# Performance work log

Hardware: AMD Instinct MI355X
Metric: run time of the kernel (lower is better)

## Reference

```python
import jax, jax.numpy as jnp
import numpy as np

NUM_CLASSES = 81
TOP_K = 200
CONF_THRESH = 0.01
NMS_THRESH = 0.45
VAR0, VAR1 = 0.1, 0.2  # SSD Config['variance']


def decode(loc, priors):
    # loc: [..., P, 4], priors: [P, 4] (cx, cy, w, h)
    cxcy = priors[:, :2] + loc[..., :2] * VAR0 * priors[:, 2:]
    wh = priors[:, 2:] * jnp.exp(loc[..., 2:] * VAR1)
    x1y1 = cxcy - wh * 0.5
    x2y2 = x1y1 + wh
    return jnp.concatenate([x1y1, x2y2], axis=-1)  # [..., P, 4] xyxy


def nms_class(boxes, scores):
    # boxes: [P, 4], scores: [P] -> [TOP_K, 5] rows of (score, x1, y1, x2, y2)
    K = TOP_K
    masked = jnp.where(scores > CONF_THRESH, scores, -jnp.inf)
    top_scores, idx = jax.lax.top_k(masked, K)          # descending
    cand = boxes[idx]                                   # [K, 4]
    valid = jnp.isfinite(top_scores)
    x1, y1, x2, y2 = cand[:, 0], cand[:, 1], cand[:, 2], cand[:, 3]
    area = (x2 - x1) * (y2 - y1)
    iw = jnp.maximum(jnp.minimum(x2[:, None], x2[None, :]) - jnp.maximum(x1[:, None], x1[None, :]), 0.0)
    ih = jnp.maximum(jnp.minimum(y2[:, None], y2[None, :]) - jnp.maximum(y1[:, None], y1[None, :]), 0.0)
    inter = iw * ih
    union = area[:, None] + area[None, :] - inter
    iou = jnp.where(union > 0, inter / jnp.where(union > 0, union, 1.0), 0.0)  # [K, K]
    ar = jnp.arange(K)

    def step(suppressed, i):
        kept = valid[i] & ~suppressed[i]
        suppressed = suppressed | (kept & (iou[i] > NMS_THRESH) & (ar > i))
        return suppressed, kept

    _, keep = jax.lax.scan(step, jnp.zeros(K, dtype=bool), ar)  # [K] bool
    rows = jnp.concatenate([jnp.where(valid, top_scores, 0.0)[:, None], cand], axis=1)  # [K, 5]
    # compact kept rows to the front (score-descending order), zeros after
    tgt = jnp.where(keep, jnp.cumsum(keep) - 1, K)
    out = jnp.zeros((K + 1, 5), rows.dtype).at[tgt].set(rows)[:K]
    return out


def detect(loc_data, conf_data, prior_data):
    boxes = decode(loc_data, prior_data)                 # [B, P, 4]
    conf = jnp.transpose(conf_data, (0, 2, 1))           # [B, C, P]
    per_image = jax.vmap(nms_class, in_axes=(None, 0))   # over classes
    out = jax.vmap(per_image, in_axes=(0, 0))(boxes, conf)  # [B, C, K, 5]
    out = out.at[:, 0].set(0.0)  # background class skipped (cl starts at 1)
    return out


def setup_inputs() -> dict:
    key = jax.random.key(0)
    k1, k2, k3 = jax.random.split(key, 3)
    B, P, C = 32, 24564, NUM_CLASSES
    loc_data = jax.random.normal(k1, (B, P, 4), dtype=jnp.float32)
    conf_data = jax.random.uniform(k2, (B, P, C), dtype=jnp.float32)
    prior_data = jax.random.uniform(k3, (P, 4), dtype=jnp.float32)
    return {"loc_data": loc_data, "conf_data": conf_data, "prior_data": prior_data}


def reference(loc_data, conf_data, prior_data):
    return detect(loc_data, conf_data, prior_data)
```

## Files before the change

kernel.cpp:

```cpp
#include <hip/hip_runtime.h>
#include <hip/hip_bf16.h>
#include <math.h>

constexpr int B_ = 32;
constexpr int P_ = 24564;
constexpr int C_ = 81;
constexpr int K_ = 200;

constexpr int NCH = 64;
constexpr int CPR = 384;
constexpr int SCAP = 1024;
constexpr int CAP  = 512;
constexpr float T_SEL = 0.9869f;

__global__ __launch_bounds__(256) void k_filter(const float* __restrict__ conf,
                                                unsigned long long* __restrict__ cand,
                                                unsigned* __restrict__ cnt,
                                                unsigned* __restrict__ bflag) {
    __shared__ unsigned long long skey[SCAP];
    __shared__ unsigned short scls[SCAP];
    __shared__ unsigned scnt[C_], sbase[C_], scnt2[C_];
    __shared__ unsigned sn;
    const int bid = blockIdx.x;
    const int b = bid / NCH, ch = bid % NCH;
    const int tid = threadIdx.x;

    for (int i = tid; i < C_; i += 256) { scnt[i] = 0; scnt2[i] = 0; }
    if (tid == 0) sn = 0;
    __syncthreads();

    const int p0 = ch * CPR;
    const int rows = min(CPR, P_ - p0);
    const float* slab = conf + ((size_t)b * P_ + (size_t)p0) * C_;
    const int n4 = rows * C_ / 4;
    for (int g = tid; g < n4; g += 256) {
        float4 v = ((const float4*)slab)[g];
        int e = g * 4;
        int c = e % C_;
        int pl = e / C_;
        float s[4] = {v.x, v.y, v.z, v.w};
#pragma unroll
        for (int j = 0; j < 4; ++j) {
            int cj = c + j, pj = pl;
            if (cj >= C_) { cj -= C_; pj += 1; }
            float sv = s[j];
            if (sv > T_SEL && cj != 0) {
                unsigned pos = atomicAdd(&sn, 1u);
                if (pos < (unsigned)SCAP) {
                    unsigned pg = (unsigned)(p0 + pj);
                    skey[pos] = ((unsigned long long)__float_as_uint(sv) << 32) | (~pg);
                    scls[pos] = (unsigned short)cj;
                    atomicAdd(&scnt[cj], 1u);
                } else {
                    bflag[b] = 1u;
                }
            }
        }
    }
    __syncthreads();
    if (tid < C_) sbase[tid] = scnt[tid] ? atomicAdd(&cnt[b * C_ + tid], scnt[tid]) : 0u;
    __syncthreads();
    const int m = (int)min(sn, (unsigned)SCAP);
    for (int i = tid; i < m; i += 256) {
        int c = scls[i];
        unsigned pos = sbase[c] + atomicAdd(&scnt2[c], 1u);
        if (pos < (unsigned)CAP)
            cand[((size_t)(b * C_ + c)) * CAP + pos] = skey[i];
    }
}

__global__ __launch_bounds__(256) void k_nms(const unsigned long long* __restrict__ cand,
                                             const unsigned* __restrict__ cnt,
                                             const unsigned* __restrict__ bflag,
                                             const float* __restrict__ conf,
                                             const float* __restrict__ loc,
                                             const float* __restrict__ prior,
                                             float* __restrict__ out) {
#pragma clang fp contract(off)
    __shared__ __align__(16) unsigned long long masks[K_][4];
    __shared__ __align__(16) unsigned long long top[256];
    __shared__ __align__(16) float4 bbox[K_];
    __shared__ float sc[K_], bar[K_];
    __shared__ unsigned char vflag[K_];
    __shared__ unsigned long long keepw[4];
    __shared__ unsigned kpre[4];
    __shared__ unsigned long long sh_prefix;
    __shared__ unsigned sh_rank, sh_cnt2, sh_cut, sh_fat;

    unsigned long long* buf = &masks[0][0];
    unsigned* rs_hist = (unsigned*)&masks[128][0];
    unsigned* rs_sf   = (unsigned*)&masks[160][0];

    const int bid = blockIdx.x;
    const int b = bid / C_, c = bid % C_;
    const int tid = threadIdx.x;
    const int lane = tid & 63;
    float* obase = out + ((size_t)(b * C_ + c)) * (K_ * 5);

    if (c == 0) {
        float4 z = make_float4(0.f, 0.f, 0.f, 0.f);
        for (int i = tid; i < K_ * 5 / 4; i += 256) ((float4*)obase)[i] = z;
        return;
    }

    const int task = b * C_ + c;
    const unsigned long long* crow = cand + (size_t)task * CAP;
    const unsigned cn = cnt[task];
    const bool fb = (bflag[b] != 0u) || (cn < (unsigned)K_) || (cn > (unsigned)CAP);

    int n;
    int snum = 0;
    bool fat = false;
    if (!fb) {
        n = (int)cn;
        const unsigned long long k1 = (tid < n)       ? crow[tid]       : 0ull;
        const unsigned long long k2 = (tid + 256 < n) ? crow[tid + 256] : 0ull;
        if (n <= 256) {
            top[tid] = k1;
            snum = n;
            __syncthreads();
        } else {
            rs_hist[tid] = 0u;
            top[tid] = 0ull;
            __syncthreads();
            atomicAdd(&rs_hist[(unsigned)((k1 >> 43) & 255ull)], 1u);
            if (tid + 256 < n)
                atomicAdd(&rs_hist[(unsigned)((k2 >> 43) & 255ull)], 1u);
            __syncthreads();
            if (tid < 64) {
                const int l = tid;
                uint4 h = *(const uint4*)&rs_hist[l * 4];
                unsigned s3 = h.w;
                unsigned s2 = h.z + s3;
                unsigned s1 = h.y + s2;
                unsigned s0 = h.x + s1;
                unsigned acc = s0;
                for (int off = 1; off < 64; off <<= 1) {
                    unsigned o = __shfl_down(acc, off, 64);
                    if (l + off < 64) acc += o;
                }
                const unsigned suf_after = acc - s0;
                unsigned long long bal = __ballot(s0 + suf_after >= (unsigned)K_);
                int hl = 63 - __builtin_clzll(bal);
                if (l == hl) {
                    int k; unsigned sufk;
                    if      (s3 + suf_after >= (unsigned)K_) { k = 3; sufk = s3 + suf_after; }
                    else if (s2 + suf_after >= (unsigned)K_) { k = 2; sufk = s2 + suf_after; }
                    else if (s1 + suf_after >= (unsigned)K_) { k = 1; sufk = s1 + suf_after; }
                    else                                     { k = 0; sufk = s0 + suf_after; }
                    sh_cut = (unsigned)(l * 4 + k);
                    sh_fat = (sufk > 256u) ? 1u : 0u;
                    sh_cnt2 = 0u;
                }
            }
            __syncthreads();
            fat = (sh_fat != 0u);
            if (!fat) {
                const unsigned cut = sh_cut;
                {
                    bool q = ((unsigned)((k1 >> 43) & 255ull) >= cut);
                    unsigned long long bal = __ballot(q);
                    unsigned pre = (unsigned)__popcll(bal & ((1ull << lane) - 1ull));
                    unsigned wb = 0;
                    if (lane == 0) {
                        unsigned cw = (unsigned)__popcll(bal);
                        if (cw) wb = atomicAdd(&sh_cnt2, cw);
                    }
                    wb = (unsigned)__shfl((int)wb, 0, 64);
                    if (q) top[wb + pre] = k1;
                }
                {
                    bool q = (tid + 256 < n) && ((unsigned)((k2 >> 43) & 255ull) >= cut);
                    unsigned long long bal = __ballot(q);
                    unsigned pre = (unsigned)__popcll(bal & ((1ull << lane) - 1ull));
                    unsigned wb = 0;
                    if (lane == 0) {
                        unsigned cw = (unsigned)__popcll(bal);
                        if (cw) wb = atomicAdd(&sh_cnt2, cw);
                    }
                    wb = (unsigned)__shfl((int)wb, 0, 64);
                    if (q) top[wb + pre] = k2;
                }
                __syncthreads();
                snum = (int)sh_cnt2;
            } else {
                buf[tid] = k1;
                buf[tid + 256] = k2;
                __syncthreads();
            }
        }
    } else {
        for (int i = tid; i < CAP; i += 256) buf[i] = 0ull;
        const float* col = conf + (size_t)b * P_ * C_ + c;
        unsigned lc = 0;
        for (int p = tid; p < P_; p += 256)
            if (col[(size_t)p * C_] > 0.01f) lc++;
        rs_sf[tid] = lc;
        __syncthreads();
        for (int off = 128; off > 0; off >>= 1) {
            if (tid < off) rs_sf[tid] += rs_sf[tid + off];
            __syncthreads();
        }
        const unsigned total = rs_sf[0];
        unsigned long long t200v = 1ull;
        if (total > (unsigned)K_) {
            if (tid == 0) { sh_prefix = 0ull; sh_rank = (unsigned)K_; }
            __syncthreads();
            for (int d = 7; d >= 0; --d) {
                rs_hist[tid] = 0;
                __syncthreads();
                const unsigned long long pref = sh_prefix;
                const unsigned rank = sh_rank;
                for (int p = tid; p < P_; p += 256) {
                    float sv = col[(size_t)p * C_];
                    if (sv > 0.01f) {
                        unsigned long long key =
                            ((unsigned long long)__float_as_uint(sv) << 32) | (~(unsigned)p);
                        bool match = (d == 7) || (((key ^ pref) >> ((d + 1) * 8)) == 0ull);
                        if (match) atomicAdd(&rs_hist[(unsigned)((key >> (d * 8)) & 255ull)], 1u);
                    }
                }
                __syncthreads();
                rs_sf[tid] = rs_hist[tid];
                __syncthreads();
                for (int off = 1; off < 256; off <<= 1) {
                    unsigned v2 = (tid + off < 256) ? rs_sf[tid + off] : 0u;
                    __syncthreads();
                    rs_sf[tid] += v2;
                    __syncthreads();
                }
                if (rs_sf[tid] >= rank && (tid == 255 || rs_sf[tid + 1] < rank)) {
                    sh_prefix = pref | ((unsigned long long)tid << (d * 8));
                    sh_rank = rank - ((tid == 255) ? 0u : rs_sf[tid + 1]);
                }
                __syncthreads();
            }
            t200v = sh_prefix;
        }
        if (tid == 0) sh_cnt2 = 0;
        __syncthreads();
        for (int p = tid; p < P_; p += 256) {
            float sv = col[(size_t)p * C_];
            if (sv > 0.01f) {
                unsigned long long key =
                    ((unsigned long long)__float_as_uint(sv) << 32) | (~(unsigned)p);
                if (key >= t200v) {
                    unsigned pos = atomicAdd(&sh_cnt2, 1u);
                    if (pos < (unsigned)CAP) buf[pos] = key;
                }
            }
        }
        __syncthreads();
        n = (int)min(sh_cnt2, (unsigned)CAP);
        top[tid] = (tid < n) ? buf[tid] : 0ull;
        snum = n;
        __syncthreads();
    }

    const int nsel = min(n, K_);

    auto decode_to = [&](unsigned long long key, int r) {
        unsigned ub = (unsigned)(key >> 32);
        unsigned p = ~((unsigned)key);
        float score = __uint_as_float(ub);
        bool v = ((ub & 0x7F800000u) != 0x7F800000u);
        const float4 l4 = ((const float4*)loc)[(size_t)b * P_ + p];
        const float4 p4 = ((const float4*)prior)[p];
        float cx = p4.x + (l4.x * 0.1f) * p4.z;
        float cy = p4.y + (l4.y * 0.1f) * p4.w;
        float w  = p4.z * expf(l4.z * 0.2f);
        float h  = p4.w * expf(l4.w * 0.2f);
        float x1 = cx - w * 0.5f;
        float y1 = cy - h * 0.5f;
        float x2 = x1 + w;
        float y2 = y1 + h;
        bbox[r] = make_float4(x1, y1, x2, y2);
        sc[r] = score;
        bar[r] = (x2 - x1) * (y2 - y1);
        vflag[r] = v ? (unsigned char)1 : (unsigned char)0;
    };

    if (!fat) {
        const unsigned long long k = top[tid];
        int r = 0;
        const int mm = (snum + 3) & ~3;
        for (int i = 0; i < mm; i += 4) {
            ulonglong2 a = *(const ulonglong2*)&top[i];
            ulonglong2 d = *(const ulonglong2*)&top[i + 2];
            r += (a.x > k) + (a.y > k) + (d.x > k) + (d.y > k);
        }
        if (k != 0ull && r < K_) decode_to(k, r);
    } else {
        const unsigned long long k1 = buf[tid];
        const unsigned long long k2 = buf[tid + 256];
        int r1 = 0, r2 = 0;
        for (int i = 0; i < CAP; i += 4) {
            ulonglong2 a = *(const ulonglong2*)&buf[i];
            ulonglong2 d = *(const ulonglong2*)&buf[i + 2];
            r1 += (a.x > k1) + (a.y > k1) + (d.x > k1) + (d.y > k1);
            r2 += (a.x > k2) + (a.y > k2) + (d.x > k2) + (d.y > k2);
        }
        if (k1 != 0ull && r1 < K_) decode_to(k1, r1);
        if (k2 != 0ull && r2 < K_) decode_to(k2, r2);
    }
    if (tid >= nsel && tid < K_) {
        bbox[tid] = make_float4(1e30f, 1e30f, 1e30f, 1e30f);
        sc[tid] = 0.f; bar[tid] = 0.f; vflag[tid] = 0;
    }
    __syncthreads();

    const double M_IOU = 0.5 * ((double)__uint_as_float(0x3EE66666u) +
                                (double)__uint_as_float(0x3EE66667u));
    const int nv = nsel;
    const int wid = tid >> 6;

    float4 jb[4]; float jar[4];
#pragma unroll
    for (int w = 0; w < 4; ++w) {
        int j = w * 64 + lane;
        bool in = (j < K_);
        jb[w]  = in ? bbox[j] : make_float4(1e30f, 1e30f, 1e30f, 1e30f);
        jar[w] = in ? bar[j] : 0.f;
    }

    for (int idx = tid; idx < K_ * 4; idx += 256) {
        int i = idx >> 2, w = idx & 3;
        if (w < (i >> 6)) masks[i][w] = 0ull;
    }
    for (int i = wid; i < nv; i += 4) {
        float4 rb = bbox[i];
        float r_ar = bar[i];
        const int w0 = i >> 6;
        const unsigned long long dmask = (0xFFFFFFFFFFFFFFFEull << (i & 63));
#pragma unroll
        for (int w = 0; w < 4; ++w) {
            if (w >= w0) {
                float xx1 = fmaxf(rb.x, jb[w].x);
                float yy1 = fmaxf(rb.y, jb[w].y);
                float xx2 = fminf(rb.z, jb[w].z);
                float yy2 = fminf(rb.w, jb[w].w);
                float iw = fmaxf(xx2 - xx1, 0.0f);
                float ih = fmaxf(yy2 - yy1, 0.0f);
                float inter = iw * ih;
                float uni = (r_ar + jar[w]) - inter;
                bool pred = (uni > 0.0f) && ((double)inter > M_IOU * (double)uni);
                unsigned long long m = __ballot(pred);
                if (w == w0) m &= dmask;
                if (lane == 0) masks[i][w] = m;
            }
        }
    }
    __syncthreads();

    if (tid < 64) {
        const int l = tid;
        unsigned long long V0 = __ballot((l       < nv) && vflag[l]);
        unsigned long long V1 = __ballot((64 + l  < nv) && vflag[64 + l]);
        unsigned long long V2 = __ballot((128 + l < nv) && vflag[128 + l]);
        unsigned long long V3 = __ballot((192 + l < nv) && vflag[192 + l]);
        auto rownz = [&](int r) -> bool {
            if (r >= nv) return false;
            return (masks[r][0] | masks[r][1] | masks[r][2] | masks[r][3]) != 0ull;
        };
        unsigned long long R0 = __ballot(rownz(l))       & V0;
        unsigned long long R1 = __ballot(rownz(64 + l))  & V1;
        unsigned long long R2 = __ballot(rownz(128 + l)) & V2;
        unsigned long long R3 = __ballot(rownz(192 + l)) & V3;

        unsigned long long S0 = 0, S1 = 0, S2 = 0, S3 = 0;
        while (true) {
            unsigned long long t;
            int i = -1;
            if ((t = R0 & ~S0) != 0ull)      i = (int)__builtin_ctzll(t);
            else if ((t = R1 & ~S1) != 0ull) i = 64 + (int)__builtin_ctzll(t);
            else if ((t = R2 & ~S2) != 0ull) i = 128 + (int)__builtin_ctzll(t);
            else if ((t = R3 & ~S3) != 0ull) i = 192 + (int)__builtin_ctzll(t);
            if (i < 0) break;
            const unsigned long long bit = 1ull << (i & 63);
            const int slot = i >> 6;
            if (slot == 0) R0 ^= bit; else if (slot == 1) R1 ^= bit;
            else if (slot == 2) R2 ^= bit; else R3 ^= bit;
            ulonglong2 m01 = *(const ulonglong2*)&masks[i][0];
            ulonglong2 m23 = *(const ulonglong2*)&masks[i][2];
            S0 |= m01.x; S1 |= m01.y; S2 |= m23.x; S3 |= m23.y;
        }
        if (l == 0) {
            unsigned long long K0 = V0 & ~S0, K1 = V1 & ~S1, K2 = V2 & ~S2, K3 = V3 & ~S3;
            keepw[0] = K0; keepw[1] = K1; keepw[2] = K2; keepw[3] = K3;
            kpre[0] = 0;
            kpre[1] = (unsigned)__popcll(K0);
            kpre[2] = kpre[1] + (unsigned)__popcll(K1);
            kpre[3] = kpre[2] + (unsigned)__popcll(K2);
        }
    }
    __syncthreads();

    if (tid < K_) {
        int w = tid >> 6, bit = tid & 63;
        if ((keepw[w] >> bit) & 1ull) {
            unsigned slot = kpre[w] + (unsigned)__popcll(keepw[w] & ((1ull << bit) - 1ull));
            float4 bb = bbox[tid];
            float* o = obase + slot * 5;
            o[0] = sc[tid]; o[1] = bb.x; o[2] = bb.y; o[3] = bb.z; o[4] = bb.w;
        }
    }
    {
        const unsigned keptTotal = kpre[3] + (unsigned)__popcll(keepw[3]);
        const int zbase = (int)keptTotal * 5;
        const int ztot = K_ * 5 - zbase;
        for (int e = tid; e < ztot; e += 256) obase[zbase + e] = 0.0f;
    }
}

extern "C" void kernel_launch(void* const* d_in, const int* in_sizes, int n_in,
                              void* d_out, int out_size, void* d_ws, size_t ws_size,
                              hipStream_t stream) {
    const float* loc   = (const float*)d_in[0];
    const float* conf  = (const float*)d_in[1];
    const float* prior = (const float*)d_in[2];
    float* out = (float*)d_out;

    char* ws = (char*)d_ws;
    const size_t candBytes = (size_t)B_ * C_ * CAP * sizeof(unsigned long long);
    unsigned long long* cand = (unsigned long long*)ws;
    unsigned* cnt   = (unsigned*)(ws + candBytes);
    unsigned* bflag = cnt + (size_t)B_ * C_;

    hipMemsetAsync(cnt, 0, (size_t)(B_ * C_ + B_) * sizeof(unsigned), stream);

    k_filter<<<B_ * NCH, 256, 0, stream>>>(conf, cand, cnt, bflag);
    k_nms   <<<B_ * C_,  256, 0, stream>>>(cand, cnt, bflag, conf, loc, prior, out);
}
```

Measured before the change: 140.7 us.

## Interleave NMS mask building with chunked suppression to skip suppressed rows

```diff
diff --git a/kernel.cpp b/kernel.cpp
--- a/kernel.cpp
+++ b/kernel.cpp
@@ -83,6 +83,7 @@
     __shared__ float sc[K_], bar[K_];
     __shared__ unsigned char vflag[K_];
     __shared__ unsigned long long keepw[4];
+    __shared__ unsigned long long Swords[4];
     __shared__ unsigned kpre[4];
     __shared__ unsigned long long sh_prefix;
     __shared__ unsigned sh_rank, sh_cnt2, sh_cut, sh_fat;
@@ -280,6 +281,7 @@
         vflag[r] = v ? (unsigned char)1 : (unsigned char)0;
     };
 
+    if (tid < 4 && !fb) Swords[tid] = 0ull;
     if (!fat) {
         const unsigned long long k = top[tid];
         int r = 0;
@@ -307,6 +309,7 @@
         bbox[tid] = make_float4(1e30f, 1e30f, 1e30f, 1e30f);
         sc[tid] = 0.f; bar[tid] = 0.f; vflag[tid] = 0;
     }
+    if (fb && tid < 4) Swords[tid] = 0ull;
     __syncthreads();
 
     const double M_IOU = 0.5 * ((double)__uint_as_float(0x3EE66666u) +
@@ -315,83 +318,82 @@
     const int wid = tid >> 6;
 
     float4 jb[4]; float jar[4];
+    unsigned long long Vw[4];
 #pragma unroll
     for (int w = 0; w < 4; ++w) {
         int j = w * 64 + lane;
         bool in = (j < K_);
         jb[w]  = in ? bbox[j] : make_float4(1e30f, 1e30f, 1e30f, 1e30f);
         jar[w] = in ? bar[j] : 0.f;
-    }
-
-    for (int idx = tid; idx < K_ * 4; idx += 256) {
-        int i = idx >> 2, w = idx & 3;
-        if (w < (i >> 6)) masks[i][w] = 0ull;
-    }
-    for (int i = wid; i < nv; i += 4) {
-        float4 rb = bbox[i];
-        float r_ar = bar[i];
-        const int w0 = i >> 6;
-        const unsigned long long dmask = (0xFFFFFFFFFFFFFFFEull << (i & 63));
+        Vw[w]  = __ballot(in && (j < nv) && vflag[j]);
+    }
+
+    unsigned long long S0 = 0, S1 = 0, S2 = 0, S3 = 0;
+    unsigned long long K0 = 0, K1r = 0, K2r = 0, K3r = 0;
+
+    const int nchunks = (nv + 63) >> 6;
+    for (int cidx = 0; cidx < nchunks; ++cidx) {
+        const int lo = cidx << 6;
+        const int hi = min(nv, lo + 64);
+        {
+            const unsigned long long act = Vw[cidx] & ~Swords[cidx];
+            for (int i = lo + wid; i < hi; i += 4) {
+                if (!((act >> (i - lo)) & 1ull)) continue;
+                float4 rb = bbox[i];
+                float r_ar = bar[i];
+                const unsigned long long dmask = (0xFFFFFFFFFFFFFFFEull << (i & 63));
 #pragma unroll
-        for (int w = 0; w < 4; ++w) {
-            if (w >= w0) {
-                float xx1 = fmaxf(rb.x, jb[w].x);
-                float yy1 = fmaxf(rb.y, jb[w].y);
-                float xx2 = fminf(rb.z, jb[w].z);
-                float yy2 = fminf(rb.w, jb[w].w);
-                float iw = fmaxf(xx2 - xx1, 0.0f);
-                float ih = fmaxf(yy2 - yy1, 0.0f);
-                float inter = iw * ih;
-                float uni = (r_ar + jar[w]) - inter;
-                bool pred = (uni > 0.0f) && ((double)inter > M_IOU * (double)uni);
-                unsigned long long m = __ballot(pred);
-                if (w == w0) m &= dmask;
-                if (lane == 0) masks[i][w] = m;
-            }
-        }
-    }
-    __syncthreads();
-
-    if (tid < 64) {
-        const int l = tid;
-        unsigned long long V0 = __ballot((l       < nv) && vflag[l]);
-        unsigned long long V1 = __ballot((64 + l  < nv) && vflag[64 + l]);
-        unsigned long long V2 = __ballot((128 + l < nv) && vflag[128 + l]);
-        unsigned long long V3 = __ballot((192 + l < nv) && vflag[192 + l]);
-        auto rownz = [&](int r) -> bool {
-            if (r >= nv) return false;
-            return (masks[r][0] | masks[r][1] | masks[r][2] | masks[r][3]) != 0ull;
-        };
-        unsigned long long R0 = __ballot(rownz(l))       & V0;
-        unsigned long long R1 = __ballot(rownz(64 + l))  & V1;
-        unsigned long long R2 = __ballot(rownz(128 + l)) & V2;
-        unsigned long long R3 = __ballot(rownz(192 + l)) & V3;
-
-        unsigned long long S0 = 0, S1 = 0, S2 = 0, S3 = 0;
-        while (true) {
-            unsigned long long t;
-            int i = -1;
-            if ((t = R0 & ~S0) != 0ull)      i = (int)__builtin_ctzll(t);
-            else if ((t = R1 & ~S1) != 0ull) i = 64 + (int)__builtin_ctzll(t);
-            else if ((t = R2 & ~S2) != 0ull) i = 128 + (int)__builtin_ctzll(t);
-            else if ((t = R3 & ~S3) != 0ull) i = 192 + (int)__builtin_ctzll(t);
-            if (i < 0) break;
-            const unsigned long long bit = 1ull << (i & 63);
-            const int slot = i >> 6;
-            if (slot == 0) R0 ^= bit; else if (slot == 1) R1 ^= bit;
-            else if (slot == 2) R2 ^= bit; else R3 ^= bit;
-            ulonglong2 m01 = *(const ulonglong2*)&masks[i][0];
-            ulonglong2 m23 = *(const ulonglong2*)&masks[i][2];
-            S0 |= m01.x; S1 |= m01.y; S2 |= m23.x; S3 |= m23.y;
-        }
-        if (l == 0) {
-            unsigned long long K0 = V0 & ~S0, K1 = V1 & ~S1, K2 = V2 & ~S2, K3 = V3 & ~S3;
-            keepw[0] = K0; keepw[1] = K1; keepw[2] = K2; keepw[3] = K3;
-            kpre[0] = 0;
-            kpre[1] = (unsigned)__popcll(K0);
-            kpre[2] = kpre[1] + (unsigned)__popcll(K1);
-            kpre[3] = kpre[2] + (unsigned)__popcll(K2);
-        }
+                for (int w = 0; w < 4; ++w) {
+                    if (w >= cidx) {
+                        float xx1 = fmaxf(rb.x, jb[w].x);
+                        float yy1 = fmaxf(rb.y, jb[w].y);
+                        float xx2 = fminf(rb.z, jb[w].z);
+                        float yy2 = fminf(rb.w, jb[w].w);
+                        float iw = fmaxf(xx2 - xx1, 0.0f);
+                        float ih = fmaxf(yy2 - yy1, 0.0f);
+                        float inter = iw * ih;
+                        float uni = (r_ar + jar[w]) - inter;
+                        bool pred = (uni > 0.0f) && ((double)inter > M_IOU * (double)uni);
+                        unsigned long long m = __ballot(pred);
+                        if (w == cidx) m &= dmask;
+                        if (lane == 0) masks[i][w] = m;
+                    }
+                }
+            }
+        }
+        __syncthreads();
+        if (tid < 64) {
+            unsigned long long Sc = (cidx == 0) ? S0 : (cidx == 1) ? S1
+                                   : (cidx == 2) ? S2 : S3;
+            unsigned long long R = Vw[cidx] & ~Sc;
+            while (R) {
+                const int bit = (int)__builtin_ctzll(R);
+                const int i = lo + bit;
+                const unsigned long long pb = 1ull << bit;
+                R ^= pb;
+                if (cidx == 0) K0 |= pb; else if (cidx == 1) K1r |= pb;
+                else if (cidx == 2) K2r |= pb; else K3r |= pb;
+                if (cidx <= 0) S0 |= masks[i][0];
+                if (cidx <= 1) S1 |= masks[i][1];
+                if (cidx <= 2) S2 |= masks[i][2];
+                S3 |= masks[i][3];
+                unsigned long long Sc2 = (cidx == 0) ? S0 : (cidx == 1) ? S1
+                                        : (cidx == 2) ? S2 : S3;
+                R &= ~Sc2;
+            }
+            if (lane == 0) {
+                Swords[0] = S0; Swords[1] = S1; Swords[2] = S2; Swords[3] = S3;
+            }
+        }
+        __syncthreads();
+    }
+
+    if (tid < 64 && lane == 0) {
+        keepw[0] = K0; keepw[1] = K1r; keepw[2] = K2r; keepw[3] = K3r;
+        kpre[0] = 0;
+        kpre[1] = (unsigned)__popcll(K0);
+        kpre[2] = kpre[1] + (unsigned)__popcll(K1r);
+        kpre[3] = kpre[2] + (unsigned)__popcll(K2r);
     }
     __syncthreads();
 
```

New measurement: 174.1 us. +23.7%, slower.
